# Kernel tuning notes

Measured on AMD Instinct MI355X. Metric: run time of the kernel, lower is better.

## Reference

```python
import jax, jax.numpy as jnp
import numpy as np

B = 512
D_IN = 64
D_MODEL = 768
DEPTH = 24
D_INNER = 1536   # expand=2 * d_model
D_STATE = 16
D_CONV = 4
DT_RANK = 48     # ceil(d_model/16)


def setup_inputs() -> dict:
    key = jax.random.key(0)
    ks = jax.random.split(key, 12)
    s = 0.02
    x_t = jax.random.normal(ks[0], (B, 1, D_IN), dtype=jnp.float32)
    in_w = jax.random.normal(ks[1], (D_MODEL, D_IN), dtype=jnp.float32) * s
    in_b = jnp.zeros((D_MODEL,), jnp.float32)
    xz_w = jax.random.normal(ks[2], (DEPTH, 2 * D_INNER, D_MODEL), dtype=jnp.float32) * s
    conv_w = jax.random.normal(ks[3], (DEPTH, D_INNER, D_CONV), dtype=jnp.float32) * s
    conv_b = jnp.zeros((DEPTH, D_INNER), jnp.float32)
    xproj_w = jax.random.normal(ks[4], (DEPTH, DT_RANK + 2 * D_STATE, D_INNER), dtype=jnp.float32) * s
    dtproj_w = jax.random.normal(ks[5], (DEPTH, D_INNER, DT_RANK), dtype=jnp.float32) * s
    # dt bias initialized so softplus(dt) ~ [1e-3, 1e-1], as in mamba_ssm
    dtproj_b = jax.random.uniform(ks[6], (DEPTH, D_INNER), minval=-4.6, maxval=-2.3)
    # A = arange(1, d_state+1) per channel -> A_log = log(A)
    A_log = jnp.broadcast_to(jnp.log(jnp.arange(1, D_STATE + 1, dtype=jnp.float32)),
                             (DEPTH, D_INNER, D_STATE)).copy()
    D = jnp.ones((DEPTH, D_INNER), jnp.float32)
    outproj_w = jax.random.normal(ks[7], (DEPTH, D_MODEL, D_INNER), dtype=jnp.float32) * s
    conv_state = jax.random.normal(ks[8], (DEPTH, B, D_INNER, D_CONV), dtype=jnp.float32) * 0.1
    ssm_state = jax.random.normal(ks[9], (DEPTH, B, D_INNER, D_STATE), dtype=jnp.float32) * 0.1
    ln_g = jnp.ones((D_MODEL,), jnp.float32)
    ln_b = jnp.zeros((D_MODEL,), jnp.float32)
    return dict(x_t=x_t, in_w=in_w, in_b=in_b, xz_w=xz_w, conv_w=conv_w, conv_b=conv_b,
                xproj_w=xproj_w, dtproj_w=dtproj_w, dtproj_b=dtproj_b, A_log=A_log, D=D,
                outproj_w=outproj_w, conv_state=conv_state, ssm_state=ssm_state,
                ln_g=ln_g, ln_b=ln_b)


def _layer_step(h, layer):
    """One Mamba selective-scan decode step for a single layer. h: (B, D_INNER*... wait (B, d_model))"""
    (xz_w, conv_w, conv_b, xproj_w, dtproj_w, dtproj_b, A_log, Dp, outproj_w, cs, ss) = layer
    xz = h @ xz_w.T                                  # (B, 2*d_inner)
    x, z = jnp.split(xz, 2, axis=-1)                 # (B, d_inner) each
    # causal conv1d cache update: shift left, append new token
    cs = jnp.concatenate([cs[..., 1:], x[..., None]], axis=-1)   # (B, d_inner, d_conv)
    x = jnp.sum(cs * conv_w[None], axis=-1) + conv_b             # (B, d_inner)
    x = jax.nn.silu(x)
    xdb = x @ xproj_w.T                              # (B, dt_rank + 2*d_state)
    dt = xdb[:, :DT_RANK] @ dtproj_w.T               # (B, d_inner)
    Bm = xdb[:, DT_RANK:DT_RANK + D_STATE]           # (B, d_state)
    C = xdb[:, DT_RANK + D_STATE:]                   # (B, d_state)
    dt = jax.nn.softplus(dt + dtproj_b)
    A = -jnp.exp(A_log)                              # (d_inner, d_state)
    dA = jnp.exp(dt[:, :, None] * A[None])           # (B, d_inner, d_state)
    ss = ss * dA + (dt * x)[:, :, None] * Bm[:, None, :]
    y = jnp.einsum('bdn,bn->bd', ss, C) + Dp * x
    y = y * jax.nn.silu(z)
    h = y @ outproj_w.T                              # (B, d_model)
    return h, None


def reference(x_t, in_w, in_b, xz_w, conv_w, conv_b, xproj_w, dtproj_w, dtproj_b,
              A_log, D, outproj_w, conv_state, ssm_state, ln_g, ln_b):
    h = x_t[:, 0, :] @ in_w.T + in_b                 # (B, d_model)
    h, _ = jax.lax.scan(_layer_step, h,
                        (xz_w, conv_w, conv_b, xproj_w, dtproj_w, dtproj_b,
                         A_log, D, outproj_w, conv_state, ssm_state))
    mu = jnp.mean(h, axis=-1, keepdims=True)
    var = jnp.var(h, axis=-1, keepdims=True)
    h = (h - mu) / jnp.sqrt(var + 1e-5) * ln_g + ln_b
    return h[:, None, :]                             # (B, 1, d_model)
```

## Files before the change

kernel.cpp:

```cpp
#include <hip/hip_runtime.h>
#include <cstdint>
#include <cstddef>

#define BATCH 512
#define D_IN 64
#define D_MODEL 768
#define DEPTH 24
#define D_INNER 1536
#define D_STATE 16
#define D_CONV 4
#define DT_RANK 48
#define XDB_DIM 80

typedef __bf16 bf16x8 __attribute__((ext_vector_type(8)));
typedef unsigned short ushortx8 __attribute__((ext_vector_type(8)));
typedef float f32x4 __attribute__((ext_vector_type(4)));
typedef unsigned short ushort_t;

__device__ __forceinline__ float sigmoidf_(float v) { return 1.f / (1.f + expf(-v)); }

__device__ __forceinline__ void split1(float f, unsigned short& h, unsigned short& l) {
    unsigned int u = __float_as_uint(f);
    unsigned int uh = u & 0xffff0000u;
    h = (unsigned short)(uh >> 16);
    float r = f - __uint_as_float(uh);
    l = (unsigned short)(__float_as_uint(r) >> 16);
}

__global__ __launch_bounds__(256) void prep_split(
    const float* __restrict__ src, ushort_t* __restrict__ hi, ushort_t* __restrict__ lo,
    long n8)
{
    long i = (long)blockIdx.x * 256 + threadIdx.x;
    const long stride = (long)gridDim.x * 256;
    for (; i < n8; i += stride) {
        float4 a = *(const float4*)(src + i * 8);
        float4 b = *(const float4*)(src + i * 8 + 4);
        float f[8] = {a.x, a.y, a.z, a.w, b.x, b.y, b.z, b.w};
        ushortx8 h, l;
#pragma unroll
        for (int j = 0; j < 8; ++j) {
            unsigned short hh, ll;
            split1(f[j], hh, ll);
            h[j] = hh; l[j] = ll;
        }
        *(ushortx8*)(hi + i * 8) = h;
        *(ushortx8*)(lo + i * 8) = l;
    }
}

template<bool CONV>
__global__ __launch_bounds__(256) void mfma_gemm2(
    const ushort_t* __restrict__ Ahi, const ushort_t* __restrict__ Alo,
    const ushort_t* __restrict__ Whi, const ushort_t* __restrict__ Wlo,
    float* __restrict__ Cout,
    float* __restrict__ Zout,
    ushort_t* __restrict__ Chi,
    ushort_t* __restrict__ Clo,
    const float* __restrict__ conv_state,
    const float* __restrict__ conv_w,
    const float* __restrict__ conv_b,
    int N, int K)
{
    __shared__ __align__(16) unsigned short As[2][64 * 64];
    __shared__ __align__(16) unsigned short Bs[2][64 * 64];

    const int t = threadIdx.x;
    const int bn0 = blockIdx.x * 64;
    const int bm0 = blockIdx.y * 64;
    const int sr = t >> 2;
    const int s0 = t & 3;
    const int lane = t & 63;
    const int wv = t >> 6;
    const int wm = wv >> 1, wn = wv & 1;
    const int ln15 = lane & 15, kq = lane >> 4;

    const ushort_t* Ah = Ahi + (size_t)(bm0 + sr) * K + s0 * 8;
    const ushort_t* Al = Alo + (size_t)(bm0 + sr) * K + s0 * 8;
    const ushort_t* Wh = Whi + (size_t)(bn0 + sr) * K + s0 * 8;
    const ushort_t* Wl = Wlo + (size_t)(bn0 + sr) * K + s0 * 8;

    f32x4 acc[2][2];
#pragma unroll
    for (int m = 0; m < 2; ++m)
#pragma unroll
        for (int n = 0; n < 2; ++n) acc[m][n] = (f32x4){0.f, 0.f, 0.f, 0.f};

    const int sw = sr & 7;
    auto stage = [&](ushortx8 hi, ushortx8 lo, unsigned short* S) {
        *(ushortx8*)&S[sr * 64 + ((s0 ^ sw) << 3)] = hi;
        *(ushortx8*)&S[sr * 64 + (((s0 + 4) ^ sw) << 3)] = lo;
    };

    const int nk = K >> 5;

    ushortx8 pah = *(const ushortx8*)Ah;
    ushortx8 pal = *(const ushortx8*)Al;
    ushortx8 pwh = *(const ushortx8*)Wh;
    ushortx8 pwl = *(const ushortx8*)Wl;
    stage(pah, pal, As[0]);
    stage(pwh, pwl, Bs[0]);

    for (int kb = 0; kb < nk; ++kb) {
        __syncthreads();
        const int cur = kb & 1;
        if (kb + 1 < nk) {
            const int ko = (kb + 1) << 5;
            pah = *(const ushortx8*)(Ah + ko);
            pal = *(const ushortx8*)(Al + ko);
            pwh = *(const ushortx8*)(Wh + ko);
            pwl = *(const ushortx8*)(Wl + ko);
        }
        bf16x8 ah[2], al[2], bh[2], bl[2];
#pragma unroll
        for (int m = 0; m < 2; ++m) {
            const int r = wm * 32 + m * 16 + ln15;
            const int base = r * 64;
            const int rs = r & 7;
            ah[m] = __builtin_bit_cast(bf16x8, *(ushortx8*)&As[cur][base + ((kq ^ rs) << 3)]);
            al[m] = __builtin_bit_cast(bf16x8, *(ushortx8*)&As[cur][base + (((kq + 4) ^ rs) << 3)]);
        }
#pragma unroll
        for (int n = 0; n < 2; ++n) {
            const int r = wn * 32 + n * 16 + ln15;
            const int base = r * 64;
            const int rs = r & 7;
            bh[n] = __builtin_bit_cast(bf16x8, *(ushortx8*)&Bs[cur][base + ((kq ^ rs) << 3)]);
            bl[n] = __builtin_bit_cast(bf16x8, *(ushortx8*)&Bs[cur][base + (((kq + 4) ^ rs) << 3)]);
        }
#pragma unroll
        for (int m = 0; m < 2; ++m)
#pragma unroll
            for (int n = 0; n < 2; ++n) {
                acc[m][n] = __builtin_amdgcn_mfma_f32_16x16x32_bf16(ah[m], bh[n], acc[m][n], 0, 0, 0);
                acc[m][n] = __builtin_amdgcn_mfma_f32_16x16x32_bf16(ah[m], bl[n], acc[m][n], 0, 0, 0);
                acc[m][n] = __builtin_amdgcn_mfma_f32_16x16x32_bf16(al[m], bh[n], acc[m][n], 0, 0, 0);
            }
        if (kb + 1 < nk) {
            stage(pah, pal, As[cur ^ 1]);
            stage(pwh, pwl, Bs[cur ^ 1]);
        }
    }

#pragma unroll
    for (int m = 0; m < 2; ++m) {
#pragma unroll
        for (int n = 0; n < 2; ++n) {
            const int col = bn0 + wn * 32 + n * 16 + ln15;
            const int row0 = bm0 + wm * 32 + m * 16 + kq * 4;
            f32x4 v = acc[m][n];
            if (CONV) {
                if (col < D_INNER) {
                    const float4 cwv = *(const float4*)(conv_w + (size_t)col * 4);
                    const float cbv = conv_b[col];
#pragma unroll
                    for (int j = 0; j < 4; ++j) {
                        const int row = row0 + j;
                        const float4 csv = *(const float4*)(conv_state + ((size_t)row * D_INNER + col) * 4);
                        float c = csv.y * cwv.x + csv.z * cwv.y + csv.w * cwv.z
                                + v[j] * cwv.w + cbv;
                        Cout[(size_t)row * D_INNER + col] = c * sigmoidf_(c);
                    }
                } else {
#pragma unroll
                    for (int j = 0; j < 4; ++j)
                        Zout[(size_t)(row0 + j) * D_INNER + (col - D_INNER)] = v[j];
                }
            } else {
#pragma unroll
                for (int j = 0; j < 4; ++j) {
                    const size_t idx = (size_t)(row0 + j) * N + col;
                    float val = v[j];
                    Cout[idx] = val;
                    unsigned short hh, ll;
                    split1(val, hh, ll);
                    Chi[idx] = hh;
                    Clo[idx] = ll;
                }
            }
        }
    }
}

template<int TM, int TN>
__global__ __launch_bounds__(256) void gemm_k(
    const float* __restrict__ A,
    const float* __restrict__ W,
    const float* __restrict__ bias,
    float* __restrict__ Cout,
    ushort_t* __restrict__ Chi, ushort_t* __restrict__ Clo,
    int M, int N, int K)
{
    constexpr int BM = 16 * TM;
    constexpr int BN = 16 * TN;
    constexpr int BK = 16;
    __shared__ float As[BK][BM + 4];
    __shared__ float Ws[BK][BN + 4];

    const int tid = threadIdx.x;
    const int tx = tid & 15;
    const int ty = tid >> 4;
    const int bn0 = blockIdx.x * BN;
    const int bm0 = blockIdx.y * BM;

    float acc[TM][TN];
#pragma unroll
    for (int i = 0; i < TM; ++i)
#pragma unroll
        for (int j = 0; j < TN; ++j) acc[i][j] = 0.f;

    for (int k0 = 0; k0 < K; k0 += BK) {
        {
            int r = tid >> 2, c = (tid & 3) << 2;
            float4 a4 = *(const float4*)(A + (size_t)(bm0 + r) * K + k0 + c);
            As[c + 0][r] = a4.x; As[c + 1][r] = a4.y;
            As[c + 2][r] = a4.z; As[c + 3][r] = a4.w;
            float4 w4 = *(const float4*)(W + (size_t)(bn0 + r) * K + k0 + c);
            Ws[c + 0][r] = w4.x; Ws[c + 1][r] = w4.y;
            Ws[c + 2][r] = w4.z; Ws[c + 3][r] = w4.w;
        }
        __syncthreads();
#pragma unroll
        for (int kk = 0; kk < BK; ++kk) {
            float af[TM], wf[TN];
#pragma unroll
            for (int i = 0; i < TM; ++i) af[i] = As[kk][ty * TM + i];
#pragma unroll
            for (int j = 0; j < TN; ++j) wf[j] = Ws[kk][tx * TN + j];
#pragma unroll
            for (int i = 0; i < TM; ++i)
#pragma unroll
                for (int j = 0; j < TN; ++j) acc[i][j] += af[i] * wf[j];
        }
        __syncthreads();
    }

#pragma unroll
    for (int i = 0; i < TM; ++i) {
        const int bb = bm0 + ty * TM + i;
#pragma unroll
        for (int j = 0; j < TN; ++j) {
            const int n = bn0 + tx * TN + j;
            float v = acc[i][j] + bias[n];
            const size_t idx = (size_t)bb * N + n;
            Cout[idx] = v;
            unsigned short hh, ll;
            split1(v, hh, ll);
            Chi[idx] = hh;
            Clo[idx] = ll;
        }
    }
}

__global__ __launch_bounds__(256) void bc_kernel(
    const float* __restrict__ x,
    const float* __restrict__ z,
    const float* __restrict__ xproj_w,
    const float* __restrict__ dtproj_w,
    const float* __restrict__ dtproj_b,
    const float* __restrict__ A_log,
    const float* __restrict__ Dp,
    const float* __restrict__ ssm,
    float* __restrict__ y,
    ushort_t* __restrict__ yhi, ushort_t* __restrict__ ylo)
{
    const int b = blockIdx.x;
    const int tid = threadIdx.x;
    __shared__ __align__(16) float xs[D_INNER];
    __shared__ float xdb[XDB_DIM];

    const float4* xrow = (const float4*)(x + (size_t)b * D_INNER);
    float4* xs4 = (float4*)xs;
    for (int i = tid; i < D_INNER / 4; i += 256) xs4[i] = xrow[i];
    __syncthreads();

    const int lane = tid & 63;
    const int wv = tid >> 6;
    for (int n = wv; n < XDB_DIM; n += 4) {
        const float4* wr = (const float4*)(xproj_w + (size_t)n * D_INNER);
        float s = 0.f;
#pragma unroll
        for (int j = 0; j < D_INNER / 4 / 64; ++j) {
            float4 w = wr[lane + 64 * j];
            float4 xv = xs4[lane + 64 * j];
            s += w.x * xv.x + w.y * xv.y + w.z * xv.z + w.w * xv.w;
        }
#pragma unroll
        for (int off = 32; off > 0; off >>= 1) s += __shfl_xor(s, off);
        if (lane == 0) xdb[n] = s;
    }
    __syncthreads();

    float Bmv[D_STATE], Cv[D_STATE];
#pragma unroll
    for (int n = 0; n < D_STATE; ++n) {
        Bmv[n] = xdb[DT_RANK + n];
        Cv[n] = xdb[DT_RANK + D_STATE + n];
    }

    for (int d = tid; d < D_INNER; d += 256) {
        const float4* dtw = (const float4*)(dtproj_w + (size_t)d * DT_RANK);
        float s = 0.f;
#pragma unroll
        for (int j = 0; j < DT_RANK / 4; ++j) {
            float4 w = dtw[j];
            s += w.x * xdb[4 * j + 0] + w.y * xdb[4 * j + 1]
               + w.z * xdb[4 * j + 2] + w.w * xdb[4 * j + 3];
        }
        s += dtproj_b[d];
        float dt = fmaxf(s, 0.f) + log1pf(expf(-fabsf(s)));
        float xv = xs[d];
        float dtx = dt * xv;

        const float4* ssp = (const float4*)(ssm + ((size_t)b * D_INNER + d) * D_STATE);
        const float4* alp = (const float4*)(A_log + (size_t)d * D_STATE);
        float yacc = 0.f;
#pragma unroll
        for (int q = 0; q < 4; ++q) {
            float4 al = alp[q];
            float4 sv = ssp[q];
            float e0 = expf(-dt * expf(al.x));
            float e1 = expf(-dt * expf(al.y));
            float e2 = expf(-dt * expf(al.z));
            float e3 = expf(-dt * expf(al.w));
            yacc += (sv.x * e0 + dtx * Bmv[4 * q + 0]) * Cv[4 * q + 0];
            yacc += (sv.y * e1 + dtx * Bmv[4 * q + 1]) * Cv[4 * q + 1];
            yacc += (sv.z * e2 + dtx * Bmv[4 * q + 2]) * Cv[4 * q + 2];
            yacc += (sv.w * e3 + dtx * Bmv[4 * q + 3]) * Cv[4 * q + 3];
        }
        yacc += Dp[d] * xv;
        float zv = z[(size_t)b * D_INNER + d];
        float out = yacc * (zv * sigmoidf_(zv));
        const size_t idx = (size_t)b * D_INNER + d;
        y[idx] = out;
        unsigned short hh, ll;
        split1(out, hh, ll);
        yhi[idx] = hh;
        ylo[idx] = ll;
    }
}

__global__ __launch_bounds__(256) void ln_kernel(
    const float* __restrict__ h, const float* __restrict__ g,
    const float* __restrict__ be, float* __restrict__ out)
{
    const int b = blockIdx.x;
    const int tid = threadIdx.x;
    float v[3];
#pragma unroll
    for (int j = 0; j < 3; ++j) v[j] = h[(size_t)b * D_MODEL + tid + j * 256];
    float s = v[0] + v[1] + v[2];
    float s2 = v[0] * v[0] + v[1] * v[1] + v[2] * v[2];
#pragma unroll
    for (int off = 32; off > 0; off >>= 1) {
        s += __shfl_xor(s, off);
        s2 += __shfl_xor(s2, off);
    }
    __shared__ float red[8];
    const int lane = tid & 63, wv = tid >> 6;
    if (lane == 0) { red[wv] = s; red[4 + wv] = s2; }
    __syncthreads();
    s = red[0] + red[1] + red[2] + red[3];
    s2 = red[4] + red[5] + red[6] + red[7];
    const float mu = s * (1.f / D_MODEL);
    const float var = s2 * (1.f / D_MODEL) - mu * mu;
    const float inv = 1.f / sqrtf(var + 1e-5f);
#pragma unroll
    for (int j = 0; j < 3; ++j) {
        int c = tid + j * 256;
        out[(size_t)b * D_MODEL + c] = (v[j] - mu) * inv * g[c] + be[c];
    }
}

extern "C" void kernel_launch(void* const* d_in, const int* in_sizes, int n_in,
                              void* d_out, int out_size, void* d_ws, size_t ws_size,
                              hipStream_t stream)
{
    const float* x_t        = (const float*)d_in[0];
    const float* in_w       = (const float*)d_in[1];
    const float* in_b       = (const float*)d_in[2];
    const float* xz_w       = (const float*)d_in[3];
    const float* conv_w     = (const float*)d_in[4];
    const float* conv_b     = (const float*)d_in[5];
    const float* xproj_w    = (const float*)d_in[6];
    const float* dtproj_w   = (const float*)d_in[7];
    const float* dtproj_b   = (const float*)d_in[8];
    const float* A_log      = (const float*)d_in[9];
    const float* Dvec       = (const float*)d_in[10];
    const float* outproj_w  = (const float*)d_in[11];
    const float* conv_state = (const float*)d_in[12];
    const float* ssm_state  = (const float*)d_in[13];
    const float* ln_g       = (const float*)d_in[14];
    const float* ln_b       = (const float*)d_in[15];

    float* ws = (float*)d_ws;
    float* h = ws;
    float* x = h + (size_t)BATCH * D_MODEL;
    float* z = x + (size_t)BATCH * D_INNER;
    float* y = z + (size_t)BATCH * D_INNER;
    ushort_t* us = (ushort_t*)(y + (size_t)BATCH * D_INNER);
    ushort_t* h_hi   = us;
    ushort_t* h_lo   = h_hi + (size_t)BATCH * D_MODEL;
    ushort_t* y_hi   = h_lo + (size_t)BATCH * D_MODEL;
    ushort_t* y_lo   = y_hi + (size_t)BATCH * D_INNER;
    ushort_t* xzw_hi = y_lo + (size_t)BATCH * D_INNER;
    ushort_t* xzw_lo = xzw_hi + (size_t)DEPTH * 2 * D_INNER * D_MODEL;
    ushort_t* opw_hi = xzw_lo + (size_t)DEPTH * 2 * D_INNER * D_MODEL;
    ushort_t* opw_lo = opw_hi + (size_t)DEPTH * D_MODEL * D_INNER;

    dim3 blk(256);

    prep_split<<<dim3(2048), blk, 0, stream>>>(
        xz_w, xzw_hi, xzw_lo, (long)DEPTH * 2 * D_INNER * D_MODEL / 8);
    prep_split<<<dim3(2048), blk, 0, stream>>>(
        outproj_w, opw_hi, opw_lo, (long)DEPTH * D_MODEL * D_INNER / 8);

    gemm_k<4, 4><<<dim3(D_MODEL / 64, BATCH / 64), blk, 0, stream>>>(
        x_t, in_w, in_b, h, h_hi, h_lo, BATCH, D_MODEL, D_IN);

    for (int l = 0; l < DEPTH; ++l) {
        const ushort_t* xzh = xzw_hi + (size_t)l * 2 * D_INNER * D_MODEL;
        const ushort_t* xzl = xzw_lo + (size_t)l * 2 * D_INNER * D_MODEL;
        const ushort_t* oph = opw_hi + (size_t)l * D_MODEL * D_INNER;
        const ushort_t* opl = opw_lo + (size_t)l * D_MODEL * D_INNER;
        const float* csl = conv_state + (size_t)l * BATCH * D_INNER * D_CONV;
        const float* cwl = conv_w + (size_t)l * D_INNER * D_CONV;
        const float* cbl = conv_b + (size_t)l * D_INNER;
        const float* xpl = xproj_w + (size_t)l * XDB_DIM * D_INNER;
        const float* dwl = dtproj_w + (size_t)l * D_INNER * DT_RANK;
        const float* dbl = dtproj_b + (size_t)l * D_INNER;
        const float* all = A_log + (size_t)l * D_INNER * D_STATE;
        const float* dpl = Dvec + (size_t)l * D_INNER;
        const float* ssl = ssm_state + (size_t)l * BATCH * D_INNER * D_STATE;

        mfma_gemm2<true><<<dim3(2 * D_INNER / 64, BATCH / 64), blk, 0, stream>>>(
            h_hi, h_lo, xzh, xzl, x, z, nullptr, nullptr,
            csl, cwl, cbl, 2 * D_INNER, D_MODEL);

        bc_kernel<<<dim3(BATCH), blk, 0, stream>>>(
            x, z, xpl, dwl, dbl, all, dpl, ssl, y, y_hi, y_lo);

        mfma_gemm2<false><<<dim3(D_MODEL / 64, BATCH / 64), blk, 0, stream>>>(
            y_hi, y_lo, oph, opl, h, nullptr, h_hi, h_lo,
            nullptr, nullptr, nullptr, D_MODEL, D_INNER);
    }

    ln_kernel<<<dim3(BATCH), blk, 0, stream>>>(h, ln_g, ln_b, (float*)d_out);
}
```

Before: 2.467 ms.

## Merge prep kernels, precompute A, batch-pair bc kernel, fuse silu(z) into GEMM

Merges the two weight-split kernels into one prep kernel that also precomputes -exp(A_log) for all layers. The per-layer scan kernel now handles two batch rows per block, so each xproj weight row is loaded once for two rows, and it uses fast __expf. silu(z) moves into the xz GEMM epilogue, and the y float output is dropped. The GEMMs use a 1D grid with a remapped block order and compile-time K, which is meant to improve L2 reuse. Fast-math exp slightly changes numerics.

```diff
diff --git a/kernel.cpp b/kernel.cpp
--- a/kernel.cpp
+++ b/kernel.cpp
@@ -17,7 +17,13 @@
 typedef float f32x4 __attribute__((ext_vector_type(4)));
 typedef unsigned short ushort_t;
 
-__device__ __forceinline__ float sigmoidf_(float v) { return 1.f / (1.f + expf(-v)); }
+#define XZW_N ((size_t)2 * D_INNER * D_MODEL)
+#define OPW_N ((size_t)D_MODEL * D_INNER)
+#define XZ_ALL ((long)DEPTH * (long)(XZW_N / 8))
+#define OP_ALL ((long)DEPTH * (long)(OPW_N / 8))
+#define AN_ALL ((long)DEPTH * D_INNER * D_STATE / 8)
+
+__device__ __forceinline__ float sigmoidf_(float v) { return 1.f / (1.f + __expf(-v)); }
 
 __device__ __forceinline__ void split1(float f, unsigned short& h, unsigned short& l) {
     unsigned int u = __float_as_uint(f);
@@ -27,51 +33,125 @@
     l = (unsigned short)(__float_as_uint(r) >> 16);
 }
 
-__global__ __launch_bounds__(256) void prep_split(
-    const float* __restrict__ src, ushort_t* __restrict__ hi, ushort_t* __restrict__ lo,
-    long n8)
-{
-    long i = (long)blockIdx.x * 256 + threadIdx.x;
+__device__ __forceinline__ void split8(const float* s, ushort_t* hi, ushort_t* lo) {
+    float4 A4 = *(const float4*)s;
+    float4 B4 = *(const float4*)(s + 4);
+    float f[8] = {A4.x, A4.y, A4.z, A4.w, B4.x, B4.y, B4.z, B4.w};
+    ushortx8 h, l;
+#pragma unroll
+    for (int j = 0; j < 8; ++j) {
+        unsigned short hh, ll;
+        split1(f[j], hh, ll);
+        h[j] = hh; l[j] = ll;
+    }
+    *(ushortx8*)hi = h;
+    *(ushortx8*)lo = l;
+}
+
+__global__ __launch_bounds__(256) void k_prep(
+    const float* __restrict__ xz_w, const float* __restrict__ op_w,
+    const float* __restrict__ A_log,
+    ushort_t* __restrict__ xzw_hi, ushort_t* __restrict__ xzw_lo,
+    ushort_t* __restrict__ opw_hi, ushort_t* __restrict__ opw_lo,
+    float* __restrict__ Aneg)
+{
+    const long total = XZ_ALL + OP_ALL + AN_ALL;
+    long g = (long)blockIdx.x * 256 + threadIdx.x;
     const long stride = (long)gridDim.x * 256;
-    for (; i < n8; i += stride) {
-        float4 a = *(const float4*)(src + i * 8);
-        float4 b = *(const float4*)(src + i * 8 + 4);
-        float f[8] = {a.x, a.y, a.z, a.w, b.x, b.y, b.z, b.w};
-        ushortx8 h, l;
-#pragma unroll
-        for (int j = 0; j < 8; ++j) {
+    for (; g < total; g += stride) {
+        if (g < XZ_ALL) {
+            split8(xz_w + g * 8, xzw_hi + g * 8, xzw_lo + g * 8);
+        } else if (g < XZ_ALL + OP_ALL) {
+            const long r = g - XZ_ALL;
+            split8(op_w + r * 8, opw_hi + r * 8, opw_lo + r * 8);
+        } else {
+            const long r = g - XZ_ALL - OP_ALL;
+            const float* s = A_log + r * 8;
+            float* d = Aneg + r * 8;
+#pragma unroll
+            for (int j = 0; j < 8; ++j) d[j] = -__expf(s[j]);
+        }
+    }
+}
+
+__global__ __launch_bounds__(256) void k_inproj(
+    const float* __restrict__ A, const float* __restrict__ W,
+    const float* __restrict__ bias,
+    ushort_t* __restrict__ Chi, ushort_t* __restrict__ Clo)
+{
+    __shared__ float As[16][68];
+    __shared__ float Ws[16][68];
+    const int tid = threadIdx.x;
+    const int tx = tid & 15, ty = tid >> 4;
+    const int bn0 = blockIdx.x * 64, bm0 = blockIdx.y * 64;
+    float acc[4][4] = {};
+    for (int k0 = 0; k0 < D_IN; k0 += 16) {
+        int r = tid >> 2, c = (tid & 3) << 2;
+        float4 a4 = *(const float4*)(A + (size_t)(bm0 + r) * D_IN + k0 + c);
+        As[c + 0][r] = a4.x; As[c + 1][r] = a4.y;
+        As[c + 2][r] = a4.z; As[c + 3][r] = a4.w;
+        float4 w4 = *(const float4*)(W + (size_t)(bn0 + r) * D_IN + k0 + c);
+        Ws[c + 0][r] = w4.x; Ws[c + 1][r] = w4.y;
+        Ws[c + 2][r] = w4.z; Ws[c + 3][r] = w4.w;
+        __syncthreads();
+#pragma unroll
+        for (int kk = 0; kk < 16; ++kk) {
+            float af[4], wf[4];
+#pragma unroll
+            for (int i = 0; i < 4; ++i) af[i] = As[kk][ty * 4 + i];
+#pragma unroll
+            for (int j = 0; j < 4; ++j) wf[j] = Ws[kk][tx * 4 + j];
+#pragma unroll
+            for (int i = 0; i < 4; ++i)
+#pragma unroll
+                for (int j = 0; j < 4; ++j) acc[i][j] += af[i] * wf[j];
+        }
+        __syncthreads();
+    }
+#pragma unroll
+    for (int i = 0; i < 4; ++i) {
+        const int bb = bm0 + ty * 4 + i;
+#pragma unroll
+        for (int j = 0; j < 4; ++j) {
+            const int n = bn0 + tx * 4 + j;
+            float v = acc[i][j] + bias[n];
+            const size_t idx = (size_t)bb * D_MODEL + n;
             unsigned short hh, ll;
-            split1(f[j], hh, ll);
-            h[j] = hh; l[j] = ll;
-        }
-        *(ushortx8*)(hi + i * 8) = h;
-        *(ushortx8*)(lo + i * 8) = l;
-    }
-}
-
-template<bool CONV>
-__global__ __launch_bounds__(256) void mfma_gemm2(
+            split1(v, hh, ll);
+            Chi[idx] = hh;
+            Clo[idx] = ll;
+        }
+    }
+}
+
+template<int MODE>
+__global__ __launch_bounds__(256) void k_gemm(
     const ushort_t* __restrict__ Ahi, const ushort_t* __restrict__ Alo,
     const ushort_t* __restrict__ Whi, const ushort_t* __restrict__ Wlo,
-    float* __restrict__ Cout,
-    float* __restrict__ Zout,
-    ushort_t* __restrict__ Chi,
-    ushort_t* __restrict__ Clo,
-    const float* __restrict__ conv_state,
-    const float* __restrict__ conv_w,
-    const float* __restrict__ conv_b,
-    int N, int K)
-{
+    float* __restrict__ xout, float* __restrict__ gout,
+    float* __restrict__ hout, ushort_t* __restrict__ Chi, ushort_t* __restrict__ Clo,
+    const float* __restrict__ conv_state, const float* __restrict__ conv_w,
+    const float* __restrict__ conv_b)
+{
+    constexpr int K = (MODE == 0) ? D_MODEL : D_INNER;
+    constexpr int nk = K / 32;
+    const int bid = blockIdx.x;
+    int c, r;
+    if (MODE == 0) {
+        c = (bid & 7) + ((bid >> 6) << 3);
+        r = (bid >> 3) & 7;
+    } else {
+        if (bid < 64) { c = bid & 7; r = bid >> 3; }
+        else { const int j = bid - 64; c = 8 + (j & 3); r = j >> 2; }
+    }
+    const int bn0 = c * 64, bm0 = r * 64;
+
     __shared__ __align__(16) unsigned short As[2][64 * 64];
     __shared__ __align__(16) unsigned short Bs[2][64 * 64];
 
     const int t = threadIdx.x;
-    const int bn0 = blockIdx.x * 64;
-    const int bm0 = blockIdx.y * 64;
-    const int sr = t >> 2;
-    const int s0 = t & 3;
-    const int lane = t & 63;
-    const int wv = t >> 6;
+    const int sr = t >> 2, s0 = t & 3;
+    const int lane = t & 63, wv = t >> 6;
     const int wm = wv >> 1, wn = wv & 1;
     const int ln15 = lane & 15, kq = lane >> 4;
 
@@ -91,8 +171,6 @@
         *(ushortx8*)&S[sr * 64 + ((s0 ^ sw) << 3)] = hi;
         *(ushortx8*)&S[sr * 64 + (((s0 + 4) ^ sw) << 3)] = lo;
     };
-
-    const int nk = K >> 5;
 
     ushortx8 pah = *(const ushortx8*)Ah;
     ushortx8 pal = *(const ushortx8*)Al;
@@ -111,20 +189,20 @@
             pwh = *(const ushortx8*)(Wh + ko);
             pwl = *(const ushortx8*)(Wl + ko);
         }
-        bf16x8 ah[2], al[2], bh[2], bl[2];
+        bf16x8 ah[2], al2[2], bh[2], bl[2];
 #pragma unroll
         for (int m = 0; m < 2; ++m) {
-            const int r = wm * 32 + m * 16 + ln15;
-            const int base = r * 64;
-            const int rs = r & 7;
-            ah[m] = __builtin_bit_cast(bf16x8, *(ushortx8*)&As[cur][base + ((kq ^ rs) << 3)]);
-            al[m] = __builtin_bit_cast(bf16x8, *(ushortx8*)&As[cur][base + (((kq + 4) ^ rs) << 3)]);
+            const int rr = wm * 32 + m * 16 + ln15;
+            const int base = rr * 64;
+            const int rs = rr & 7;
+            ah[m]  = __builtin_bit_cast(bf16x8, *(ushortx8*)&As[cur][base + ((kq ^ rs) << 3)]);
+            al2[m] = __builtin_bit_cast(bf16x8, *(ushortx8*)&As[cur][base + (((kq + 4) ^ rs) << 3)]);
         }
 #pragma unroll
         for (int n = 0; n < 2; ++n) {
-            const int r = wn * 32 + n * 16 + ln15;
-            const int base = r * 64;
-            const int rs = r & 7;
+            const int rr = wn * 32 + n * 16 + ln15;
+            const int base = rr * 64;
+            const int rs = rr & 7;
             bh[n] = __builtin_bit_cast(bf16x8, *(ushortx8*)&Bs[cur][base + ((kq ^ rs) << 3)]);
             bl[n] = __builtin_bit_cast(bf16x8, *(ushortx8*)&Bs[cur][base + (((kq + 4) ^ rs) << 3)]);
         }
@@ -132,9 +210,9 @@
         for (int m = 0; m < 2; ++m)
 #pragma unroll
             for (int n = 0; n < 2; ++n) {
-                acc[m][n] = __builtin_amdgcn_mfma_f32_16x16x32_bf16(ah[m], bh[n], acc[m][n], 0, 0, 0);
-                acc[m][n] = __builtin_amdgcn_mfma_f32_16x16x32_bf16(ah[m], bl[n], acc[m][n], 0, 0, 0);
-                acc[m][n] = __builtin_amdgcn_mfma_f32_16x16x32_bf16(al[m], bh[n], acc[m][n], 0, 0, 0);
+                acc[m][n] = __builtin_amdgcn_mfma_f32_16x16x32_bf16(ah[m],  bh[n], acc[m][n], 0, 0, 0);
+                acc[m][n] = __builtin_amdgcn_mfma_f32_16x16x32_bf16(ah[m],  bl[n], acc[m][n], 0, 0, 0);
+                acc[m][n] = __builtin_amdgcn_mfma_f32_16x16x32_bf16(al2[m], bh[n], acc[m][n], 0, 0, 0);
             }
         if (kb + 1 < nk) {
             stage(pah, pal, As[cur ^ 1]);
@@ -149,7 +227,7 @@
             const int col = bn0 + wn * 32 + n * 16 + ln15;
             const int row0 = bm0 + wm * 32 + m * 16 + kq * 4;
             f32x4 v = acc[m][n];
-            if (CONV) {
+            if (MODE == 0) {
                 if (col < D_INNER) {
                     const float4 cwv = *(const float4*)(conv_w + (size_t)col * 4);
                     const float cbv = conv_b[col];
@@ -157,21 +235,23 @@
                     for (int j = 0; j < 4; ++j) {
                         const int row = row0 + j;
                         const float4 csv = *(const float4*)(conv_state + ((size_t)row * D_INNER + col) * 4);
-                        float c = csv.y * cwv.x + csv.z * cwv.y + csv.w * cwv.z
-                                + v[j] * cwv.w + cbv;
-                        Cout[(size_t)row * D_INNER + col] = c * sigmoidf_(c);
+                        float cc = csv.y * cwv.x + csv.z * cwv.y + csv.w * cwv.z
+                                 + v[j] * cwv.w + cbv;
+                        xout[(size_t)row * D_INNER + col] = cc * sigmoidf_(cc);
                     }
                 } else {
 #pragma unroll
-                    for (int j = 0; j < 4; ++j)
-                        Zout[(size_t)(row0 + j) * D_INNER + (col - D_INNER)] = v[j];
+                    for (int j = 0; j < 4; ++j) {
+                        float zv = v[j];
+                        gout[(size_t)(row0 + j) * D_INNER + (col - D_INNER)] = zv * sigmoidf_(zv);
+                    }
                 }
             } else {
 #pragma unroll
                 for (int j = 0; j < 4; ++j) {
-                    const size_t idx = (size_t)(row0 + j) * N + col;
+                    const size_t idx = (size_t)(row0 + j) * D_MODEL + col;
                     float val = v[j];
-                    Cout[idx] = val;
+                    hout[idx] = val;
                     unsigned short hh, ll;
                     split1(val, hh, ll);
                     Chi[idx] = hh;
@@ -182,167 +262,104 @@
     }
 }
 
-template<int TM, int TN>
-__global__ __launch_bounds__(256) void gemm_k(
-    const float* __restrict__ A,
-    const float* __restrict__ W,
-    const float* __restrict__ bias,
-    float* __restrict__ Cout,
-    ushort_t* __restrict__ Chi, ushort_t* __restrict__ Clo,
-    int M, int N, int K)
-{
-    constexpr int BM = 16 * TM;
-    constexpr int BN = 16 * TN;
-    constexpr int BK = 16;
-    __shared__ float As[BK][BM + 4];
-    __shared__ float Ws[BK][BN + 4];
-
+__global__ __launch_bounds__(256) void k_bc(
+    const float* __restrict__ x, const float* __restrict__ g,
+    const float* __restrict__ xproj_w, const float* __restrict__ dtproj_w,
+    const float* __restrict__ dtproj_b, const float* __restrict__ Aneg_l,
+    const float* __restrict__ Dp, const float* __restrict__ ssm,
+    ushort_t* __restrict__ yhi, ushort_t* __restrict__ ylo)
+{
+    __shared__ __align__(16) float xs0[D_INNER];
+    __shared__ __align__(16) float xs1[D_INNER];
+    __shared__ float xdb0[XDB_DIM];
+    __shared__ float xdb1[XDB_DIM];
     const int tid = threadIdx.x;
-    const int tx = tid & 15;
-    const int ty = tid >> 4;
-    const int bn0 = blockIdx.x * BN;
-    const int bm0 = blockIdx.y * BM;
-
-    float acc[TM][TN];
-#pragma unroll
-    for (int i = 0; i < TM; ++i)
-#pragma unroll
-        for (int j = 0; j < TN; ++j) acc[i][j] = 0.f;
-
-    for (int k0 = 0; k0 < K; k0 += BK) {
-        {
-            int r = tid >> 2, c = (tid & 3) << 2;
-            float4 a4 = *(const float4*)(A + (size_t)(bm0 + r) * K + k0 + c);
-            As[c + 0][r] = a4.x; As[c + 1][r] = a4.y;
-            As[c + 2][r] = a4.z; As[c + 3][r] = a4.w;
-            float4 w4 = *(const float4*)(W + (size_t)(bn0 + r) * K + k0 + c);
-            Ws[c + 0][r] = w4.x; Ws[c + 1][r] = w4.y;
-            Ws[c + 2][r] = w4.z; Ws[c + 3][r] = w4.w;
-        }
-        __syncthreads();
-#pragma unroll
-        for (int kk = 0; kk < BK; ++kk) {
-            float af[TM], wf[TN];
-#pragma unroll
-            for (int i = 0; i < TM; ++i) af[i] = As[kk][ty * TM + i];
-#pragma unroll
-            for (int j = 0; j < TN; ++j) wf[j] = Ws[kk][tx * TN + j];
-#pragma unroll
-            for (int i = 0; i < TM; ++i)
-#pragma unroll
-                for (int j = 0; j < TN; ++j) acc[i][j] += af[i] * wf[j];
-        }
-        __syncthreads();
-    }
-
-#pragma unroll
-    for (int i = 0; i < TM; ++i) {
-        const int bb = bm0 + ty * TM + i;
-#pragma unroll
-        for (int j = 0; j < TN; ++j) {
-            const int n = bn0 + tx * TN + j;
-            float v = acc[i][j] + bias[n];
-            const size_t idx = (size_t)bb * N + n;
-            Cout[idx] = v;
-            unsigned short hh, ll;
-            split1(v, hh, ll);
-            Chi[idx] = hh;
-            Clo[idx] = ll;
-        }
-    }
-}
-
-__global__ __launch_bounds__(256) void bc_kernel(
-    const float* __restrict__ x,
-    const float* __restrict__ z,
-    const float* __restrict__ xproj_w,
-    const float* __restrict__ dtproj_w,
-    const float* __restrict__ dtproj_b,
-    const float* __restrict__ A_log,
-    const float* __restrict__ Dp,
-    const float* __restrict__ ssm,
-    float* __restrict__ y,
-    ushort_t* __restrict__ yhi, ushort_t* __restrict__ ylo)
-{
-    const int b = blockIdx.x;
-    const int tid = threadIdx.x;
-    __shared__ __align__(16) float xs[D_INNER];
-    __shared__ float xdb[XDB_DIM];
-
-    const float4* xrow = (const float4*)(x + (size_t)b * D_INNER);
-    float4* xs4 = (float4*)xs;
-    for (int i = tid; i < D_INNER / 4; i += 256) xs4[i] = xrow[i];
+    const int b0 = blockIdx.x * 2, b1 = b0 + 1;
+
+    {
+        const float4* xr0 = (const float4*)(x + (size_t)b0 * D_INNER);
+        const float4* xr1 = (const float4*)(x + (size_t)b1 * D_INNER);
+        float4* d0 = (float4*)xs0; float4* d1 = (float4*)xs1;
+        for (int i = tid; i < D_INNER / 4; i += 256) { d0[i] = xr0[i]; d1[i] = xr1[i]; }
+    }
     __syncthreads();
 
-    const int lane = tid & 63;
-    const int wv = tid >> 6;
+    const int lane = tid & 63, wv = tid >> 6;
+    const float4* xs40 = (const float4*)xs0;
+    const float4* xs41 = (const float4*)xs1;
     for (int n = wv; n < XDB_DIM; n += 4) {
         const float4* wr = (const float4*)(xproj_w + (size_t)n * D_INNER);
-        float s = 0.f;
+        float s0 = 0.f, s1 = 0.f;
 #pragma unroll
         for (int j = 0; j < D_INNER / 4 / 64; ++j) {
             float4 w = wr[lane + 64 * j];
-            float4 xv = xs4[lane + 64 * j];
-            s += w.x * xv.x + w.y * xv.y + w.z * xv.z + w.w * xv.w;
-        }
-#pragma unroll
-        for (int off = 32; off > 0; off >>= 1) s += __shfl_xor(s, off);
-        if (lane == 0) xdb[n] = s;
+            float4 u = xs40[lane + 64 * j];
+            float4 q = xs41[lane + 64 * j];
+            s0 += w.x * u.x + w.y * u.y + w.z * u.z + w.w * u.w;
+            s1 += w.x * q.x + w.y * q.y + w.z * q.z + w.w * q.w;
+        }
+#pragma unroll
+        for (int off = 32; off > 0; off >>= 1) { s0 += __shfl_xor(s0, off); s1 += __shfl_xor(s1, off); }
+        if (lane == 0) { xdb0[n] = s0; xdb1[n] = s1; }
     }
     __syncthreads();
 
-    float Bmv[D_STATE], Cv[D_STATE];
-#pragma unroll
-    for (int n = 0; n < D_STATE; ++n) {
-        Bmv[n] = xdb[DT_RANK + n];
-        Cv[n] = xdb[DT_RANK + D_STATE + n];
+    float B0[16], C0[16], B1[16], C1[16];
+#pragma unroll
+    for (int n = 0; n < 16; ++n) {
+        B0[n] = xdb0[DT_RANK + n]; C0[n] = xdb0[DT_RANK + 16 + n];
+        B1[n] = xdb1[DT_RANK + n]; C1[n] = xdb1[DT_RANK + 16 + n];
     }
 
     for (int d = tid; d < D_INNER; d += 256) {
         const float4* dtw = (const float4*)(dtproj_w + (size_t)d * DT_RANK);
-        float s = 0.f;
+        float s0 = 0.f, s1 = 0.f;
 #pragma unroll
         for (int j = 0; j < DT_RANK / 4; ++j) {
             float4 w = dtw[j];
-            s += w.x * xdb[4 * j + 0] + w.y * xdb[4 * j + 1]
-               + w.z * xdb[4 * j + 2] + w.w * xdb[4 * j + 3];
-        }
-        s += dtproj_b[d];
-        float dt = fmaxf(s, 0.f) + log1pf(expf(-fabsf(s)));
-        float xv = xs[d];
-        float dtx = dt * xv;
-
-        const float4* ssp = (const float4*)(ssm + ((size_t)b * D_INNER + d) * D_STATE);
-        const float4* alp = (const float4*)(A_log + (size_t)d * D_STATE);
-        float yacc = 0.f;
+            s0 += w.x * xdb0[4*j] + w.y * xdb0[4*j+1] + w.z * xdb0[4*j+2] + w.w * xdb0[4*j+3];
+            s1 += w.x * xdb1[4*j] + w.y * xdb1[4*j+1] + w.z * xdb1[4*j+2] + w.w * xdb1[4*j+3];
+        }
+        const float bb = dtproj_b[d];
+        s0 += bb; s1 += bb;
+        float dt0 = fmaxf(s0, 0.f) + log1pf(__expf(-fabsf(s0)));
+        float dt1 = fmaxf(s1, 0.f) + log1pf(__expf(-fabsf(s1)));
+        const float xv0 = xs0[d], xv1 = xs1[d];
+        const float dtx0 = dt0 * xv0, dtx1 = dt1 * xv1;
+        const float4* anp = (const float4*)(Aneg_l + (size_t)d * D_STATE);
+        const float4* sp0 = (const float4*)(ssm + ((size_t)b0 * D_INNER + d) * D_STATE);
+        const float4* sp1 = (const float4*)(ssm + ((size_t)b1 * D_INNER + d) * D_STATE);
+        float y0 = 0.f, y1 = 0.f;
 #pragma unroll
         for (int q = 0; q < 4; ++q) {
-            float4 al = alp[q];
-            float4 sv = ssp[q];
-            float e0 = expf(-dt * expf(al.x));
-            float e1 = expf(-dt * expf(al.y));
-            float e2 = expf(-dt * expf(al.z));
-            float e3 = expf(-dt * expf(al.w));
-            yacc += (sv.x * e0 + dtx * Bmv[4 * q + 0]) * Cv[4 * q + 0];
-            yacc += (sv.y * e1 + dtx * Bmv[4 * q + 1]) * Cv[4 * q + 1];
-            yacc += (sv.z * e2 + dtx * Bmv[4 * q + 2]) * Cv[4 * q + 2];
-            yacc += (sv.w * e3 + dtx * Bmv[4 * q + 3]) * Cv[4 * q + 3];
-        }
-        yacc += Dp[d] * xv;
-        float zv = z[(size_t)b * D_INNER + d];
-        float out = yacc * (zv * sigmoidf_(zv));
-        const size_t idx = (size_t)b * D_INNER + d;
-        y[idx] = out;
+            float4 an = anp[q];
+            float4 u = sp0[q];
+            float4 w = sp1[q];
+            float e;
+            e = __expf(dt0 * an.x); y0 += (u.x * e + dtx0 * B0[4*q+0]) * C0[4*q+0];
+            e = __expf(dt0 * an.y); y0 += (u.y * e + dtx0 * B0[4*q+1]) * C0[4*q+1];
+            e = __expf(dt0 * an.z); y0 += (u.z * e + dtx0 * B0[4*q+2]) * C0[4*q+2];
+            e = __expf(dt0 * an.w); y0 += (u.w * e + dtx0 * B0[4*q+3]) * C0[4*q+3];
+            e = __expf(dt1 * an.x); y1 += (w.x * e + dtx1 * B1[4*q+0]) * C1[4*q+0];
+            e = __expf(dt1 * an.y); y1 += (w.y * e + dtx1 * B1[4*q+1]) * C1[4*q+1];
+            e = __expf(dt1 * an.z); y1 += (w.z * e + dtx1 * B1[4*q+2]) * C1[4*q+2];
+            e = __expf(dt1 * an.w); y1 += (w.w * e + dtx1 * B1[4*q+3]) * C1[4*q+3];
+        }
+        const float dv = Dp[d];
+        y0 += dv * xv0; y1 += dv * xv1;
+        const float o0 = y0 * g[(size_t)b0 * D_INNER + d];
+        const float o1 = y1 * g[(size_t)b1 * D_INNER + d];
         unsigned short hh, ll;
-        split1(out, hh, ll);
-        yhi[idx] = hh;
-        ylo[idx] = ll;
-    }
-}
-
-__global__ __launch_bounds__(256) void ln_kernel(
-    const float* __restrict__ h, const float* __restrict__ g,
-    const float* __restrict__ be, float* __restrict__ out)
+        split1(o0, hh, ll);
+        yhi[(size_t)b0 * D_INNER + d] = hh; ylo[(size_t)b0 * D_INNER + d] = ll;
+        split1(o1, hh, ll);
+        yhi[(size_t)b1 * D_INNER + d] = hh; ylo[(size_t)b1 * D_INNER + d] = ll;
+    }
+}
+
+__global__ __launch_bounds__(256) void k_ln(
+    const float* __restrict__ h, const float* __restrict__ gam,
+    const float* __restrict__ bet, float* __restrict__ out)
 {
     const int b = blockIdx.x;
     const int tid = threadIdx.x;
@@ -368,7 +385,7 @@
 #pragma unroll
     for (int j = 0; j < 3; ++j) {
         int c = tid + j * 256;
-        out[(size_t)b * D_MODEL + c] = (v[j] - mu) * inv * g[c] + be[c];
+        out[(size_t)b * D_MODEL + c] = (v[j] - mu) * inv * gam[c] + bet[c];
     }
 }
 
@@ -394,56 +411,52 @@
     const float* ln_b       = (const float*)d_in[15];
 
     float* ws = (float*)d_ws;
-    float* h = ws;
-    float* x = h + (size_t)BATCH * D_MODEL;
-    float* z = x + (size_t)BATCH * D_INNER;
-    float* y = z + (size_t)BATCH * D_INNER;
-    ushort_t* us = (ushort_t*)(y + (size_t)BATCH * D_INNER);
-    ushort_t* h_hi   = us;
-    ushort_t* h_lo   = h_hi + (size_t)BATCH * D_MODEL;
-    ushort_t* y_hi   = h_lo + (size_t)BATCH * D_MODEL;
-    ushort_t* y_lo   = y_hi + (size_t)BATCH * D_INNER;
+    float* h    = ws;
+    float* x    = h + (size_t)BATCH * D_MODEL;
+    float* g    = x + (size_t)BATCH * D_INNER;
+    float* Aneg = g + (size_t)BATCH * D_INNER;
+    ushort_t* h_hi = (ushort_t*)(Aneg + (size_t)DEPTH * D_INNER * D_STATE);
+    ushort_t* h_lo = h_hi + (size_t)BATCH * D_MODEL;
+    ushort_t* y_hi = h_lo + (size_t)BATCH * D_MODEL;
+    ushort_t* y_lo = y_hi + (size_t)BATCH * D_INNER;
     ushort_t* xzw_hi = y_lo + (size_t)BATCH * D_INNER;
-    ushort_t* xzw_lo = xzw_hi + (size_t)DEPTH * 2 * D_INNER * D_MODEL;
-    ushort_t* opw_hi = xzw_lo + (size_t)DEPTH * 2 * D_INNER * D_MODEL;
-    ushort_t* opw_lo = opw_hi + (size_t)DEPTH * D_MODEL * D_INNER;
+    ushort_t* xzw_lo = xzw_hi + (size_t)DEPTH * XZW_N;
+    ushort_t* opw_hi = xzw_lo + (size_t)DEPTH * XZW_N;
+    ushort_t* opw_lo = opw_hi + (size_t)DEPTH * OPW_N;
 
     dim3 blk(256);
 
-    prep_split<<<dim3(2048), blk, 0, stream>>>(
-        xz_w, xzw_hi, xzw_lo, (long)DEPTH * 2 * D_INNER * D_MODEL / 8);
-    prep_split<<<dim3(2048), blk, 0, stream>>>(
-        outproj_w, opw_hi, opw_lo, (long)DEPTH * D_MODEL * D_INNER / 8);
-
-    gemm_k<4, 4><<<dim3(D_MODEL / 64, BATCH / 64), blk, 0, stream>>>(
-        x_t, in_w, in_b, h, h_hi, h_lo, BATCH, D_MODEL, D_IN);
+    k_prep<<<dim3(2048), blk, 0, stream>>>(
+        xz_w, outproj_w, A_log, xzw_hi, xzw_lo, opw_hi, opw_lo, Aneg);
+
+    k_inproj<<<dim3(12, 8), blk, 0, stream>>>(x_t, in_w, in_b, h_hi, h_lo);
 
     for (int l = 0; l < DEPTH; ++l) {
-        const ushort_t* xzh = xzw_hi + (size_t)l * 2 * D_INNER * D_MODEL;
-        const ushort_t* xzl = xzw_lo + (size_t)l * 2 * D_INNER * D_MODEL;
-        const ushort_t* oph = opw_hi + (size_t)l * D_MODEL * D_INNER;
-        const ushort_t* opl = opw_lo + (size_t)l * D_MODEL * D_INNER;
+        const ushort_t* xzh = xzw_hi + (size_t)l * XZW_N;
+        const ushort_t* xzl = xzw_lo + (size_t)l * XZW_N;
+        const ushort_t* oph = opw_hi + (size_t)l * OPW_N;
+        const ushort_t* opl = opw_lo + (size_t)l * OPW_N;
         const float* csl = conv_state + (size_t)l * BATCH * D_INNER * D_CONV;
         const float* cwl = conv_w + (size_t)l * D_INNER * D_CONV;
         const float* cbl = conv_b + (size_t)l * D_INNER;
         const float* xpl = xproj_w + (size_t)l * XDB_DIM * D_INNER;
         const float* dwl = dtproj_w + (size_t)l * D_INNER * DT_RANK;
         const float* dbl = dtproj_b + (size_t)l * D_INNER;
-        const float* all = A_log + (size_t)l * D_INNER * D_STATE;
+        const float* anl = Aneg + (size_t)l * D_INNER * D_STATE;
         const float* dpl = Dvec + (size_t)l * D_INNER;
         const float* ssl = ssm_state + (size_t)l * BATCH * D_INNER * D_STATE;
 
-        mfma_gemm2<true><<<dim3(2 * D_INNER / 64, BATCH / 64), blk, 0, stream>>>(
-            h_hi, h_lo, xzh, xzl, x, z, nullptr, nullptr,
-            csl, cwl, cbl, 2 * D_INNER, D_MODEL);
-
-        bc_kernel<<<dim3(BATCH), blk, 0, stream>>>(
-            x, z, xpl, dwl, dbl, all, dpl, ssl, y, y_hi, y_lo);
-
-        mfma_gemm2<false><<<dim3(D_MODEL / 64, BATCH / 64), blk, 0, stream>>>(
-            y_hi, y_lo, oph, opl, h, nullptr, h_hi, h_lo,
-            nullptr, nullptr, nullptr, D_MODEL, D_INNER);
-    }
-
-    ln_kernel<<<dim3(BATCH), blk, 0, stream>>>(h, ln_g, ln_b, (float*)d_out);
-}
+        k_gemm<0><<<dim3(384), blk, 0, stream>>>(
+            h_hi, h_lo, xzh, xzl, x, g, nullptr, nullptr, nullptr,
+            csl, cwl, cbl);
+
+        k_bc<<<dim3(256), blk, 0, stream>>>(
+            x, g, xpl, dwl, dbl, anl, dpl, ssl, y_hi, y_lo);
+
+        k_gemm<1><<<dim3(96), blk, 0, stream>>>(
+            y_hi, y_lo, oph, opl, nullptr, nullptr, h, h_hi, h_lo,
+            nullptr, nullptr, nullptr);
+    }
+
+    k_ln<<<dim3(BATCH), blk, 0, stream>>>(h, ln_g, ln_b, (float*)d_out);
+}
```

After: 2.498 ms. No clear change (+1.3%).
